# Kernel optimization log

Measured on AMD Instinct MI355X. Metric: run time of the kernel, lower is better.

## Reference

```python
import jax, jax.numpy as jnp
import numpy as np

RH, RW = 40, 64          # render image height/width
SAM_HW = 64              # SAM ViT-H feature map spatial size
FEAT_DIM = 17            # voxel_feature_dim
GAUSSIAN_SEM_WEIGHT = 1.0


def nearest_resize(x, oh, ow):
    # torch F.interpolate mode='nearest': idx = floor(out_idx * in/out)
    ih, iw = x.shape[-2], x.shape[-1]
    ri = jnp.floor(jnp.arange(oh) * (ih / oh)).astype(jnp.int32)
    ci = jnp.floor(jnp.arange(ow) * (iw / ow)).astype(jnp.int32)
    return x[..., ri, :][..., ci]


def bilinear_resize(x, oh, ow):
    # torch bilinear, align_corners=False (half-pixel centers)
    ih, iw = x.shape[-2], x.shape[-1]
    def axis(isz, osz):
        src = (jnp.arange(osz, dtype=x.dtype) + 0.5) * (isz / osz) - 0.5
        i0 = jnp.clip(jnp.floor(src), 0, isz - 1).astype(jnp.int32)
        i1 = jnp.clip(i0 + 1, 0, isz - 1)
        w = jnp.clip(src - i0.astype(x.dtype), 0.0, 1.0)
        return i0, i1, w
    r0, r1, wr = axis(ih, oh)
    c0, c1, wc = axis(iw, ow)
    xr = x[..., r0, :] * (1 - wr)[:, None] + x[..., r1, :] * wr[:, None]
    return xr[..., c0] * (1 - wc) + xr[..., c1] * wc


def quat_to_rot(q):  # q: [N,4] normalized (w,x,y,z)
    w, x, y, z = q[:, 0], q[:, 1], q[:, 2], q[:, 3]
    R = jnp.stack([
        1 - 2 * (y * y + z * z), 2 * (x * y - w * z), 2 * (x * z + w * y),
        2 * (x * y + w * z), 1 - 2 * (x * x + z * z), 2 * (y * z - w * x),
        2 * (x * z - w * y), 2 * (y * z + w * x), 1 - 2 * (x * x + y * y)], -1)
    return R.reshape(-1, 3, 3)


def sam_proj(x, W1, b1, g1, be1, W2, b2, g2, be2, W3, b3):
    # Linear -> LayerNorm -> LeakyReLU (x2) -> Linear, all on last dim
    def ln(h, g, b):
        mu = h.mean(-1, keepdims=True)
        var = ((h - mu) ** 2).mean(-1, keepdims=True)
        return (h - mu) / jnp.sqrt(var + 1e-5) * g + b
    h = jax.nn.leaky_relu(ln(x @ W1.T + b1, g1, be1), 0.01)
    h = jax.nn.leaky_relu(ln(h @ W2.T + b2, g2, be2), 0.01)
    return h @ W3.T + b3


def render_feature_map(xyz, feats, opac, scal, quat, vm, intr):
    # Differentiable EWA Gaussian-splat feature rasterizer (3DGS-style math).
    N = xyz.shape[0]
    Rw, t = vm[:3, :3], vm[:3, 3]
    cam = xyz @ Rw.T + t                      # [N,3] camera coords
    x, y, z = cam[:, 0], cam[:, 1], cam[:, 2]
    fx, fy, cx, cy = intr[0], intr[1], intr[2], intr[3]
    zc = jnp.maximum(z, 1e-3)
    u = fx * x / zc + cx
    v = fy * y / zc + cy
    # 3D covariance Sigma = R S S^T R^T, transformed to camera then projected
    Rq = quat_to_rot(quat)
    M = Rq * scal[:, None, :]
    cov3 = M @ jnp.swapaxes(M, 1, 2)          # [N,3,3]
    covw = jnp.einsum('ij,njk,lk->nil', Rw, cov3, Rw)
    inv_z = 1.0 / zc
    zero = jnp.zeros_like(z)
    J = jnp.stack([
        jnp.stack([fx * inv_z, zero, -fx * x * inv_z ** 2], -1),
        jnp.stack([zero, fy * inv_z, -fy * y * inv_z ** 2], -1)], 1)  # [N,2,3]
    cov2 = jnp.einsum('nij,njk,nlk->nil', J, covw, J)
    a = cov2[:, 0, 0] + 0.3
    bq = cov2[:, 0, 1]
    cc = cov2[:, 1, 1] + 0.3
    det = a * cc - bq * bq
    A, Bc, Cc = cc / det, -bq / det, a / det   # conic (inverse 2D cov)
    xx, yy = jnp.meshgrid(jnp.arange(RW, dtype=xyz.dtype), jnp.arange(RH, dtype=xyz.dtype))
    px, py = xx.reshape(-1), yy.reshape(-1)    # [P]
    dx = u[:, None] - px[None, :]              # [N,P]
    dy = v[:, None] - py[None, :]
    power = -0.5 * (A[:, None] * dx * dx + Cc[:, None] * dy * dy) - Bc[:, None] * dx * dy
    alpha = jnp.minimum(0.99, opac * jnp.exp(jnp.minimum(power, 0.0)))
    alpha = alpha * (z > 0.2).astype(alpha.dtype)[:, None]
    # depth-sorted alpha compositing
    order = jnp.argsort(z)
    a_s = alpha[order]                         # [N,P]
    f_s = feats[order]                         # [N,C]
    T = jnp.concatenate([jnp.ones((1, a_s.shape[1]), a_s.dtype),
                         jnp.cumprod(1.0 - a_s, axis=0)[:-1]], axis=0)
    out = jnp.einsum('np,nc->cp', a_s * T, f_s)  # white_background=False -> bg 0
    return out.reshape(FEAT_DIM, RH, RW)


def _forward(voxel_feats, opacity, sam_embd, sam_features, sam_masks, viewmat,
             intrins, pc_xyz, scales, rots, W1, b1, g1, be1, W2, b2, g2, be2, W3, b3):
    B, C = viewmat.shape[0], viewmat.shape[1]
    scal = jnp.exp(scales)
    quat = rots / jnp.linalg.norm(rots, axis=-1, keepdims=True)
    proj = lambda x: sam_proj(x, W1, b1, g1, be1, W2, b2, g2, be2, W3, b3)
    loss_batch = 0.0
    for b in range(B):
        vf = voxel_feats[b].reshape(-1, FEAT_DIM)
        op = opacity[b].reshape(-1, 1)
        loss_c = 0.0
        for c in range(C):
            fmap = render_feature_map(pc_xyz, vf, op, scal, quat, viewmat[b, c], intrins[b, c])
            # use_sam: L1 between rendered map and projected SAM embedding
            se = nearest_resize(sam_embd[b, c], RH, RW)          # [256,RH,RW]
            sed = proj(se.transpose(1, 2, 0))                    # [RH,RW,17]
            loss_c = loss_c + jnp.abs(fmap.transpose(1, 2, 0) - sed).mean()
            # SAM mask contrastive loss
            sf = sam_features[b, c]                              # [256,64,64]
            ldf = proj(sf.reshape(256, -1).T).T.reshape(FEAT_DIM, SAM_HW, SAM_HW)
            masks = sam_masks[b, c]                              # [M,200,200]
            lsm = nearest_resize(masks, SAM_HW, SAM_HW)          # [M,64,64]
            proto = jnp.einsum('mhw,chw->mc', lsm, ldf)
            proto = proto / jnp.maximum(lsm.sum((1, 2)), 1e-6)[:, None]
            prob = jax.nn.sigmoid(jnp.einsum('mc,chw->mhw', proto, fmap))
            frm = bilinear_resize(masks, RH, RW)
            frm = jnp.where(frm <= 0.5, 0.0, frm)
            bce = frm * jnp.log(prob + 1e-8) + (1 - frm) * jnp.log(1 - prob + 1e-8)
            loss_c = loss_c - bce.mean()
        loss_batch = loss_batch + loss_c / C
    return loss_batch / B * GAUSSIAN_SEM_WEIGHT


def setup_inputs() -> dict:
    key = jax.random.key(0)
    ks = jax.random.split(key, 10)
    vs = 2.0
    gx1 = np.arange(-40.0, 40.0 + vs - 0.1, vs)
    gx = (gx1[:40] + gx1[1:41]) / 2
    gy = gx.copy()
    gz1 = np.arange(-2.4, 13.6 + vs - 0.1, vs)
    gz = (gz1[:8] + gz1[1:9]) / 2
    X, Y, Z = np.meshgrid(gx, gy, gz, indexing='ij')
    pc_xyz = np.stack([X, Y, Z], -1).reshape(-1, 3).astype(np.float32)
    N = pc_xyz.shape[0]  # 12800
    # regular grid: 3-NN mean squared dist = vs^2 -> scales = log(sqrt(vs^2))
    scales = np.full((N, 3), np.log(vs), np.float32)
    rots = np.zeros((N, 4), np.float32); rots[:, 0] = 1.0
    vm = np.zeros((1, 2, 4, 4), np.float32)
    vm[0, :, 0, 0] = vm[0, :, 1, 1] = vm[0, :, 2, 2] = vm[0, :, 3, 3] = 1.0
    vm[0, 0, :3, 3] = [0.0, 0.0, 60.0]
    vm[0, 1, :3, 3] = [2.0, -1.0, 62.0]
    intr = np.tile(np.array([32.0, 20.0, 32.0, 20.0], np.float32), (1, 2, 1))
    inp = {
        'voxel_feats': jax.random.normal(ks[0], (1, N, 17), jnp.float32) * 0.5,
        'opacity': jax.random.uniform(ks[1], (1, N, 1), jnp.float32) * 0.1,
        'sam_embd': jax.random.normal(ks[2], (1, 2, 256, 64, 64), jnp.float32),
        'sam_features': jax.random.normal(ks[3], (1, 2, 256, 64, 64), jnp.float32),
        'sam_masks': (jax.random.uniform(ks[4], (1, 2, 16, 200, 200)) < 0.3).astype(jnp.float32),
        'viewmat': jnp.asarray(vm), 'intrins': jnp.asarray(intr),
        'pc_xyz': jnp.asarray(pc_xyz), 'scales': jnp.asarray(scales), 'rots': jnp.asarray(rots),
        'W1': jax.random.normal(ks[5], (64, 256), jnp.float32) * 0.05,
        'b1': jnp.zeros((64,), jnp.float32),
        'g1': jnp.ones((64,), jnp.float32), 'be1': jnp.zeros((64,), jnp.float32),
        'W2': jax.random.normal(ks[6], (64, 64), jnp.float32) * 0.1,
        'b2': jnp.zeros((64,), jnp.float32),
        'g2': jnp.ones((64,), jnp.float32), 'be2': jnp.zeros((64,), jnp.float32),
        'W3': jax.random.normal(ks[7], (17, 64), jnp.float32) * 0.1,
        'b3': jnp.zeros((17,), jnp.float32),
    }
    return inp


def reference(voxel_feats, opacity, sam_embd, sam_features, sam_masks, viewmat,
              intrins, pc_xyz, scales, rots, W1, b1, g1, be1, W2, b2, g2, be2, W3, b3):
    return _forward(voxel_feats, opacity, sam_embd, sam_features, sam_masks, viewmat,
                    intrins, pc_xyz, scales, rots, W1, b1, g1, be1, W2, b2, g2, be2, W3, b3)
```

## Files before the change

### kernel.cpp

```cpp
#include <hip/hip_runtime.h>
#include <math.h>

#define NPTS   12800
#define P_PIX  2560
#define NC     128
#define CHUNK  100
#define NRG    10
#define RANK_CHUNK 800
#define RT     4
#define MLP_PITCH 264

typedef short short8 __attribute__((ext_vector_type(8)));
typedef float f32x4 __attribute__((ext_vector_type(4)));
typedef float f32x2 __attribute__((ext_vector_type(2)));

__device__ __forceinline__ unsigned short f2bf(float f) {
    unsigned int u = __float_as_uint(f);
    u += 0x7fffu + ((u >> 16) & 1u);
    return (unsigned short)(u >> 16);
}

__device__ __forceinline__ float pack2h(float a, float b) {
    union { float f; _Float16 h[2]; } c;
    c.h[0] = (_Float16)a; c.h[1] = (_Float16)b;
    return c.f;
}
__device__ __forceinline__ float2 unpk2h(float w) {
    union { float f; _Float16 h[2]; } c; c.f = w;
    return make_float2((float)c.h[0], (float)c.h[1]);
}

__global__ __launch_bounds__(256) void prep_kernel(
    const float* __restrict__ xyz, const float* __restrict__ scales,
    const float* __restrict__ rots, const float* __restrict__ opacity,
    const float* __restrict__ viewmat, const float* __restrict__ intrins,
    unsigned long long* __restrict__ keys,
    float* __restrict__ pu, float* __restrict__ pv, float* __restrict__ prad,
    float* __restrict__ phA, float* __restrict__ phC, float* __restrict__ pnB,
    float* __restrict__ pop, int* __restrict__ rnk, float* __restrict__ out, int N) {
    int cam = blockIdx.y;
    int i = blockIdx.x * 256 + threadIdx.x;
    if (i >= N) return;
    int idx = cam * N + i;
    rnk[idx] = 0;
    if (idx == 0) out[0] = 0.0f;
    const float* vm = viewmat + cam * 16;
    const float* it = intrins + cam * 4;
    float fx = it[0], fy = it[1], cx = it[2], cy = it[3];
    float R00 = vm[0], R01 = vm[1], R02 = vm[2], t0 = vm[3];
    float R10 = vm[4], R11 = vm[5], R12 = vm[6], t1 = vm[7];
    float R20 = vm[8], R21 = vm[9], R22 = vm[10], t2 = vm[11];
    float X = xyz[i * 3], Y = xyz[i * 3 + 1], Z = xyz[i * 3 + 2];
    float x = R00 * X + R01 * Y + R02 * Z + t0;
    float y = R10 * X + R11 * Y + R12 * Z + t1;
    float z = R20 * X + R21 * Y + R22 * Z + t2;
    float zc = fmaxf(z, 0.001f);
    float iz = 1.0f / zc;
    float u = fx * x * iz + cx;
    float v = fy * y * iz + cy;
    float qw = rots[i * 4], qx = rots[i * 4 + 1], qy = rots[i * 4 + 2], qz = rots[i * 4 + 3];
    float qn = 1.0f / sqrtf(qw * qw + qx * qx + qy * qy + qz * qz);
    qw *= qn; qx *= qn; qy *= qn; qz *= qn;
    float s0 = expf(scales[i * 3]), s1 = expf(scales[i * 3 + 1]), s2 = expf(scales[i * 3 + 2]);
    float Rq[3][3] = {
        {1 - 2 * (qy * qy + qz * qz), 2 * (qx * qy - qw * qz), 2 * (qx * qz + qw * qy)},
        {2 * (qx * qy + qw * qz), 1 - 2 * (qx * qx + qz * qz), 2 * (qy * qz - qw * qx)},
        {2 * (qx * qz - qw * qy), 2 * (qy * qz + qw * qx), 1 - 2 * (qx * qx + qy * qy)}};
    float M[3][3];
    #pragma unroll
    for (int r = 0; r < 3; ++r) { M[r][0] = Rq[r][0] * s0; M[r][1] = Rq[r][1] * s1; M[r][2] = Rq[r][2] * s2; }
    float c3[3][3];
    #pragma unroll
    for (int a = 0; a < 3; ++a)
        #pragma unroll
        for (int b = 0; b < 3; ++b)
            c3[a][b] = M[a][0] * M[b][0] + M[a][1] * M[b][1] + M[a][2] * M[b][2];
    float Rw[3][3] = {{R00, R01, R02}, {R10, R11, R12}, {R20, R21, R22}};
    float Wt[3][3];
    #pragma unroll
    for (int a = 0; a < 3; ++a)
        #pragma unroll
        for (int b = 0; b < 3; ++b)
            Wt[a][b] = Rw[a][0] * c3[0][b] + Rw[a][1] * c3[1][b] + Rw[a][2] * c3[2][b];
    float cw[3][3];
    #pragma unroll
    for (int a = 0; a < 3; ++a)
        #pragma unroll
        for (int b = 0; b < 3; ++b)
            cw[a][b] = Wt[a][0] * Rw[b][0] + Wt[a][1] * Rw[b][1] + Wt[a][2] * Rw[b][2];
    float j00 = fx * iz, j02 = -fx * x * iz * iz;
    float j11 = fy * iz, j12 = -fy * y * iz * iz;
    float c00 = j00 * j00 * cw[0][0] + 2.0f * j00 * j02 * cw[0][2] + j02 * j02 * cw[2][2];
    float c01 = j00 * j11 * cw[0][1] + j00 * j12 * cw[0][2] + j02 * j11 * cw[2][1] + j02 * j12 * cw[2][2];
    float c11 = j11 * j11 * cw[1][1] + 2.0f * j11 * j12 * cw[1][2] + j12 * j12 * cw[2][2];
    float a = c00 + 0.3f, bq = c01, cc = c11 + 0.3f;
    float det = a * cc - bq * bq;
    float A = cc / det, Bc = -bq / det, Cc = a / det;
    float lmin = 0.5f * ((A + Cc) - sqrtf((A - Cc) * (A - Cc) + 4.0f * Bc * Bc));
    lmin = fmaxf(lmin, 1e-20f);
    float opv = (z > 0.2f) ? opacity[i] : 0.0f;
    float rad = -1.0f;
    if (opv > 0.0f) {
        float tcut = logf(opv) + 18.42f;
        if (tcut > 0.0f) rad = sqrtf(2.0f * tcut / lmin);
    }
    pu[idx] = u; pv[idx] = v; prad[idx] = rad;
    phA[idx] = -0.5f * A; phC[idx] = -0.5f * Cc; pnB[idx] = -Bc;
    pop[idx] = opv;
    unsigned int zb = __float_as_uint(z);
    zb = (zb & 0x80000000u) ? ~zb : (zb | 0x80000000u);
    keys[idx] = ((unsigned long long)zb << 32) | (unsigned int)i;
}

__global__ __launch_bounds__(256) void rank_kernel(const unsigned long long* __restrict__ keys,
                                                   int* __restrict__ rnk, int N) {
    __shared__ unsigned long long sk[RANK_CHUNK];
    int cam = blockIdx.z;
    const unsigned long long* K = keys + (size_t)cam * N;
    int jbase = blockIdx.y * RANK_CHUNK;
    int jcnt = min(RANK_CHUNK, N - jbase);
    for (int t = threadIdx.x; t < jcnt; t += 256) sk[t] = K[jbase + t];
    __syncthreads();
    int i0 = blockIdx.x * (256 * RT) + threadIdx.x;
    unsigned long long ki[RT];
    int cnt[RT];
    #pragma unroll
    for (int t = 0; t < RT; ++t) {
        int i = i0 + t * 256;
        ki[t] = (i < N) ? K[i] : 0xFFFFFFFFFFFFFFFFull;
        cnt[t] = 0;
    }
    #pragma unroll 4
    for (int j = 0; j < jcnt; ++j) {
        unsigned long long kj = sk[j];
        #pragma unroll
        for (int t = 0; t < RT; ++t) cnt[t] += (kj < ki[t]) ? 1 : 0;
    }
    #pragma unroll
    for (int t = 0; t < RT; ++t) {
        int i = i0 + t * 256;
        if (i < N && cnt[t]) atomicAdd(rnk + (size_t)cam * N + i, cnt[t]);
    }
}

__global__ __launch_bounds__(256) void scatter_kernel(
    const int* __restrict__ rnk,
    const float* __restrict__ pu, const float* __restrict__ pv, const float* __restrict__ prad,
    const float* __restrict__ phA, const float* __restrict__ phC, const float* __restrict__ pnB,
    const float* __restrict__ pop,
    const float* __restrict__ feats, float* __restrict__ rec, float2* __restrict__ vr, int N) {
    int cam = blockIdx.y;
    int i = blockIdx.x * 256 + threadIdx.x;
    if (i >= N) return;
    int idx = cam * N + i;
    int r = rnk[idx];
    float* d = rec + ((size_t)cam * N + r) * 16;
    d[0] = pu[idx]; d[1] = pv[idx];
    d[2] = pack2h(phA[idx], phC[idx]);
    d[3] = pack2h(pnB[idx], pop[idx]);
    const float* f = feats + (size_t)i * 17;
    #pragma unroll
    for (int j = 0; j < 8; ++j) d[4 + j] = pack2h(f[2 * j], f[2 * j + 1]);
    d[12] = pack2h(f[16], 0.0f);
    d[13] = 0.0f; d[14] = 0.0f; d[15] = 0.0f;
    vr[(size_t)cam * N + r] = make_float2(pv[idx], prad[idx]);
}

__global__ __launch_bounds__(256) void expand_kernel(const float2* __restrict__ vr,
                                                     const float* __restrict__ rec,
                                                     float* __restrict__ cstream,
                                                     int* __restrict__ cnts, int N) {
    int gid = blockIdx.x * 4 + (threadIdx.x >> 6);
    int lane = threadIdx.x & 63;
    int cam = gid / (NC * NRG);
    int rem = gid - cam * (NC * NRG);
    int ch = rem / NRG, rg = rem - ch * NRG;
    const float2* V = vr + (size_t)cam * N + ch * CHUNK;
    const float4* R = (const float4*)(rec + ((size_t)cam * N + ch * CHUNK) * 16);
    float4* S = (float4*)(cstream + (size_t)gid * CHUNK * 16);
    float cy = (float)(rg * 4) + 1.5f;
    int cnt = 0;
    #pragma unroll
    for (int g = 0; g < CHUNK; g += 64) {
        int n = g + lane;
        bool pass = false;
        if (n < CHUNK) {
            float2 t = V[n];
            pass = fabsf(t.x - cy) <= t.y + 2.01f;
        }
        unsigned long long mask = __ballot(pass);
        int pre = __popcll(mask & ((1ull << lane) - 1ull));
        if (pass) {
            int pos = cnt + pre;
            S[pos * 4 + 0] = R[n * 4 + 0];
            S[pos * 4 + 1] = R[n * 4 + 1];
            S[pos * 4 + 2] = R[n * 4 + 2];
            S[pos * 4 + 3] = R[n * 4 + 3];
        }
        cnt += __popcll(mask);
    }
    if (lane == 0) cnts[gid] = cnt;
}

__global__ __launch_bounds__(64) void splat_kernel(const float* __restrict__ cstream,
                                                   const int* __restrict__ cnts,
                                                   float* __restrict__ partT,
                                                   unsigned short* __restrict__ partS, int N) {
    __shared__ __align__(16) float4 sRec[CHUNK * 4];
    int rg = blockIdx.x, ch = blockIdx.y, cam = blockIdx.z;
    int lane = threadIdx.x;
    int lid = (cam * NC + ch) * NRG + rg;
    int cnt = cnts[lid];
    const float4* S = (const float4*)(cstream + (size_t)lid * CHUNK * 16);
    for (int t = lane; t < cnt * 4; t += 64) sRec[t] = S[t];
    __syncthreads();
    int r0 = rg * 4;
    float px = (float)lane, py0 = (float)r0;
    float T0 = 1.0f, T1 = 1.0f, T2 = 1.0f, T3 = 1.0f;
    f32x2 accA[17], accB[17];
    #pragma unroll
    for (int c = 0; c < 17; ++c) { accA[c] = (f32x2){0.f, 0.f}; accB[c] = (f32x2){0.f, 0.f}; }
    const float* sRf = (const float*)sRec;
    for (int i = 0; i < cnt; ++i) {
        const float4* rp = sRec + i * 4;
        float4 q0 = rp[0];
        float2 g0 = unpk2h(q0.z);
        float2 g1 = unpk2h(q0.w);
        float dx = q0.x - px;
        float dy = q0.y - py0;
        float ta = (g0.x * dx) * dx;
        float tb = g1.x * dx;
        float h2 = g0.y + g0.y;
        float p0 = fmaf(dy, fmaf(g0.y, dy, tb), ta);
        float e = fmaf(-h2, dy, g0.y - tb);
        float p1 = p0 + e; e += h2;
        float p2 = p1 + e; e += h2;
        float p3 = p2 + e;
        float a0 = fminf(0.99f, g1.y * __expf(fminf(p0, 0.0f)));
        float a1 = fminf(0.99f, g1.y * __expf(fminf(p1, 0.0f)));
        float a2 = fminf(0.99f, g1.y * __expf(fminf(p2, 0.0f)));
        float a3 = fminf(0.99f, g1.y * __expf(fminf(p3, 0.0f)));
        f32x2 wA = (f32x2){a0 * T0, a1 * T1};
        f32x2 wB = (f32x2){a2 * T2, a3 * T3};
        T0 = fmaf(-T0, a0, T0); T1 = fmaf(-T1, a1, T1);
        T2 = fmaf(-T2, a2, T2); T3 = fmaf(-T3, a3, T3);
        float4 q1 = rp[1], q2 = rp[2];
        float q3x = sRf[i * 16 + 12];
        float2 f01 = unpk2h(q1.x), f23 = unpk2h(q1.y), f45 = unpk2h(q1.z), f67 = unpk2h(q1.w);
        float2 f89 = unpk2h(q2.x), fab = unpk2h(q2.y), fcd = unpk2h(q2.z), fef = unpk2h(q2.w);
        float2 fg_ = unpk2h(q3x);
        accA[0]  += wA * f01.x;  accB[0]  += wB * f01.x;
        accA[1]  += wA * f01.y;  accB[1]  += wB * f01.y;
        accA[2]  += wA * f23.x;  accB[2]  += wB * f23.x;
        accA[3]  += wA * f23.y;  accB[3]  += wB * f23.y;
        accA[4]  += wA * f45.x;  accB[4]  += wB * f45.x;
        accA[5]  += wA * f45.y;  accB[5]  += wB * f45.y;
        accA[6]  += wA * f67.x;  accB[6]  += wB * f67.x;
        accA[7]  += wA * f67.y;  accB[7]  += wB * f67.y;
        accA[8]  += wA * f89.x;  accB[8]  += wB * f89.x;
        accA[9]  += wA * f89.y;  accB[9]  += wB * f89.y;
        accA[10] += wA * fab.x;  accB[10] += wB * fab.x;
        accA[11] += wA * fab.y;  accB[11] += wB * fab.y;
        accA[12] += wA * fcd.x;  accB[12] += wB * fcd.x;
        accA[13] += wA * fcd.y;  accB[13] += wB * fcd.y;
        accA[14] += wA * fef.x;  accB[14] += wB * fef.x;
        accA[15] += wA * fef.y;  accB[15] += wB * fef.y;
        accA[16] += wA * fg_.x;  accB[16] += wB * fg_.x;
    }
    size_t cbase = (size_t)(cam * NC + ch);
    size_t p0i = (size_t)r0 * 64 + lane;
    partT[cbase * P_PIX + p0i]       = T0;
    partT[cbase * P_PIX + p0i + 64]  = T1;
    partT[cbase * P_PIX + p0i + 128] = T2;
    partT[cbase * P_PIX + p0i + 192] = T3;
    _Float16* pS = (_Float16*)partS;
    #pragma unroll
    for (int c = 0; c < 17; ++c) {
        size_t b = (cbase * 17 + c) * P_PIX + p0i;
        pS[b]       = (_Float16)accA[c][0];
        pS[b + 64]  = (_Float16)accA[c][1];
        pS[b + 128] = (_Float16)accB[c][0];
        pS[b + 192] = (_Float16)accB[c][1];
    }
}

__global__ __launch_bounds__(256) void combine_kernel(const float* __restrict__ partT,
                                                      const unsigned short* __restrict__ partS,
                                                      float* __restrict__ fmap) {
    int idx = blockIdx.x * 256 + threadIdx.x;
    if (idx >= 2 * 17 * P_PIX) return;
    int p = idx % P_PIX;
    int rem = idx / P_PIX;
    int c = rem % 17;
    int cam = rem / 17;
    const _Float16* pS = (const _Float16*)partS;
    float acc = 0.0f, Tp = 1.0f;
    #pragma unroll 8
    for (int k = 0; k < NC; ++k) {
        size_t cb = (size_t)(cam * NC + k);
        float Tk = partT[cb * P_PIX + p];
        float S = (float)pS[(cb * 17 + c) * P_PIX + p];
        acc = fmaf(Tp, S, acc);
        Tp *= Tk;
    }
    fmap[((size_t)cam * 17 + c) * P_PIX + p] = acc;
}

__global__ __launch_bounds__(256, 2) void mlp_kernel(
    const float* __restrict__ embd, const float* __restrict__ sfeat,
    const float* __restrict__ W1, const float* __restrict__ b1,
    const float* __restrict__ g1, const float* __restrict__ be1,
    const float* __restrict__ W2, const float* __restrict__ b2,
    const float* __restrict__ g2, const float* __restrict__ be2,
    const float* __restrict__ W3, const float* __restrict__ b3,
    float* __restrict__ sed, float* __restrict__ ldf) {
    __shared__ __align__(16) unsigned short smem[2 * 64 * MLP_PITCH];
    unsigned short* sX = smem;
    unsigned short* sW = smem + 64 * MLP_PITCH;
    int tid = threadIdx.x, lane = tid & 63, wv = tid >> 6;
    int m = lane & 15, kq = lane >> 4, q4 = kq * 4;
    int tile = blockIdx.x;
    const float* xbase;
    if (tile < 80) {
        int cam = tile / 40; int r = tile - cam * 40;
        int ri = (r * 8) / 5;
        xbase = embd + (size_t)cam * 256 * 4096 + ri * 64;
    } else {
        int tt = tile - 80; int cam = tt >> 6;
        xbase = sfeat + (size_t)cam * 256 * 4096 + (tt & 63) * 64;
    }
    const float4* xf4 = (const float4*)xbase;
    for (int idx = tid; idx < 4096; idx += 256) {
        int k = idx >> 4, q = idx & 15;
        float4 xv = xf4[(size_t)k * 1024 + q];
        int r = q * 4;
        sX[(r + 0) * MLP_PITCH + k] = f2bf(xv.x);
        sX[(r + 1) * MLP_PITCH + k] = f2bf(xv.y);
        sX[(r + 2) * MLP_PITCH + k] = f2bf(xv.z);
        sX[(r + 3) * MLP_PITCH + k] = f2bf(xv.w);
    }
    const float4* wf4 = (const float4*)W1;
    for (int idx = tid; idx < 4096; idx += 256) {
        float4 wvv = wf4[idx];
        int n = idx >> 6, kk = (idx & 63) * 4;
        uint2 pk;
        pk.x = (unsigned int)f2bf(wvv.x) | ((unsigned int)f2bf(wvv.y) << 16);
        pk.y = (unsigned int)f2bf(wvv.z) | ((unsigned int)f2bf(wvv.w) << 16);
        *(uint2*)&sW[n * MLP_PITCH + kk] = pk;
    }
    float b1v[4], g1v[4], be1v[4], b2v[4], g2v[4], be2v[4];
    #pragma unroll
    for (int nt = 0; nt < 4; ++nt) {
        int c = nt * 16 + m;
        b1v[nt] = b1[c]; g1v[nt] = g1[c]; be1v[nt] = be1[c];
        b2v[nt] = b2[c]; g2v[nt] = g2[c]; be2v[nt] = be2[c];
    }
    __syncthreads();
    f32x4 acc[4];
    #pragma unroll
    for (int nt = 0; nt < 4; ++nt) acc[nt] = (f32x4){0.f, 0.f, 0.f, 0.f};
    const unsigned short* aptr = sX + (wv * 16 + m) * MLP_PITCH + kq * 8;
    const unsigned short* bptr = sW + m * MLP_PITCH + kq * 8;
    #pragma unroll
    for (int ks = 0; ks < 8; ++ks) {
        short8 af = *(const short8*)(aptr + ks * 32);
        #pragma unroll
        for (int nt = 0; nt < 4; ++nt) {
            short8 bf = *(const short8*)(bptr + nt * 16 * MLP_PITCH + ks * 32);
            acc[nt] = __builtin_amdgcn_mfma_f32_16x16x32_bf16(af, bf, acc[nt], 0, 0, 0);
        }
    }
    __syncthreads();
    unsigned short* hbuf  = smem + wv * 16 * 72;
    unsigned short* hbuf2 = smem + (4 + wv) * 16 * 72;
    unsigned short* W2b = sW;
    unsigned short* W3b = sW + 64 * 72;
    for (int i = tid; i < 4096; i += 256)
        W2b[(i >> 6) * 72 + (i & 63)] = f2bf(W2[i]);
    for (int i = tid; i < 2048; i += 256) {
        int n = i >> 6, k = i & 63;
        W3b[n * 72 + k] = (n < 17) ? f2bf(W3[n * 64 + k]) : 0;
    }
    #pragma unroll
    for (int rg = 0; rg < 4; ++rg) {
        float h0 = acc[0][rg] + b1v[0], h1 = acc[1][rg] + b1v[1];
        float h2 = acc[2][rg] + b1v[2], h3 = acc[3][rg] + b1v[3];
        float s = (h0 + h1) + (h2 + h3);
        s += __shfl_xor(s, 1); s += __shfl_xor(s, 2);
        s += __shfl_xor(s, 4); s += __shfl_xor(s, 8);
        float mu = s * (1.0f / 64.0f);
        float d0 = h0 - mu, d1 = h1 - mu, d2 = h2 - mu, d3 = h3 - mu;
        float vs = (d0 * d0 + d1 * d1) + (d2 * d2 + d3 * d3);
        vs += __shfl_xor(vs, 1); vs += __shfl_xor(vs, 2);
        vs += __shfl_xor(vs, 4); vs += __shfl_xor(vs, 8);
        float rstd = 1.0f / sqrtf(vs * (1.0f / 64.0f) + 1e-5f);
        float hn0 = d0 * rstd * g1v[0] + be1v[0]; hn0 = fmaxf(hn0, 0.01f * hn0);
        float hn1 = d1 * rstd * g1v[1] + be1v[1]; hn1 = fmaxf(hn1, 0.01f * hn1);
        float hn2 = d2 * rstd * g1v[2] + be1v[2]; hn2 = fmaxf(hn2, 0.01f * hn2);
        float hn3 = d3 * rstd * g1v[3] + be1v[3]; hn3 = fmaxf(hn3, 0.01f * hn3);
        int rr = (q4 + rg) * 72 + m;
        hbuf[rr] = f2bf(hn0); hbuf[rr + 16] = f2bf(hn1);
        hbuf[rr + 32] = f2bf(hn2); hbuf[rr + 48] = f2bf(hn3);
    }
    __syncthreads();
    f32x4 acc2[4];
    #pragma unroll
    for (int nt = 0; nt < 4; ++nt) acc2[nt] = (f32x4){0.f, 0.f, 0.f, 0.f};
    const unsigned short* a2p = hbuf + m * 72 + kq * 8;
    #pragma unroll
    for (int ks = 0; ks < 2; ++ks) {
        short8 af = *(const short8*)(a2p + ks * 32);
        #pragma unroll
        for (int nt = 0; nt < 4; ++nt) {
            short8 bf = *(const short8*)(W2b + (nt * 16 + m) * 72 + kq * 8 + ks * 32);
            acc2[nt] = __builtin_amdgcn_mfma_f32_16x16x32_bf16(af, bf, acc2[nt], 0, 0, 0);
        }
    }
    #pragma unroll
    for (int rg = 0; rg < 4; ++rg) {
        float h0 = acc2[0][rg] + b2v[0], h1 = acc2[1][rg] + b2v[1];
        float h2 = acc2[2][rg] + b2v[2], h3 = acc2[3][rg] + b2v[3];
        float s = (h0 + h1) + (h2 + h3);
        s += __shfl_xor(s, 1); s += __shfl_xor(s, 2);
        s += __shfl_xor(s, 4); s += __shfl_xor(s, 8);
        float mu = s * (1.0f / 64.0f);
        float d0 = h0 - mu, d1 = h1 - mu, d2 = h2 - mu, d3 = h3 - mu;
        float vs = (d0 * d0 + d1 * d1) + (d2 * d2 + d3 * d3);
        vs += __shfl_xor(vs, 1); vs += __shfl_xor(vs, 2);
        vs += __shfl_xor(vs, 4); vs += __shfl_xor(vs, 8);
        float rstd = 1.0f / sqrtf(vs * (1.0f / 64.0f) + 1e-5f);
        float hn0 = d0 * rstd * g2v[0] + be2v[0]; hn0 = fmaxf(hn0, 0.01f * hn0);
        float hn1 = d1 * rstd * g2v[1] + be2v[1]; hn1 = fmaxf(hn1, 0.01f * hn1);
        float hn2 = d2 * rstd * g2v[2] + be2v[2]; hn2 = fmaxf(hn2, 0.01f * hn2);
        float hn3 = d3 * rstd * g2v[3] + be2v[3]; hn3 = fmaxf(hn3, 0.01f * hn3);
        int rr = (q4 + rg) * 72 + m;
        hbuf2[rr] = f2bf(hn0); hbuf2[rr + 16] = f2bf(hn1);
        hbuf2[rr + 32] = f2bf(hn2); hbuf2[rr + 48] = f2bf(hn3);
    }
    f32x4 acc3[2];
    acc3[0] = (f32x4){0.f, 0.f, 0.f, 0.f};
    acc3[1] = (f32x4){0.f, 0.f, 0.f, 0.f};
    const unsigned short* a3p = hbuf2 + m * 72 + kq * 8;
    #pragma unroll
    for (int ks = 0; ks < 2; ++ks) {
        short8 af = *(const short8*)(a3p + ks * 32);
        #pragma unroll
        for (int nt = 0; nt < 2; ++nt) {
            short8 bf = *(const short8*)(W3b + (nt * 16 + m) * 72 + kq * 8 + ks * 32);
            acc3[nt] = __builtin_amdgcn_mfma_f32_16x16x32_bf16(af, bf, acc3[nt], 0, 0, 0);
        }
    }
    #pragma unroll
    for (int nt = 0; nt < 2; ++nt) {
        int c = nt * 16 + m;
        if (c < 17) {
            float b3v = b3[c];
            #pragma unroll
            for (int rg = 0; rg < 4; ++rg) {
                int row = tile * 64 + wv * 16 + q4 + rg;
                float val = acc3[nt][rg] + b3v;
                if (row < 5120) {
                    int cam = row / 2560; int p = row - cam * 2560;
                    sed[((size_t)cam * 2560 + p) * 17 + c] = val;
                } else {
                    int rr = row - 5120; int cam = rr >> 12; int t = rr & 4095;
                    ldf[((size_t)cam * 17 + c) * 4096 + t] = val;
                }
            }
        }
    }
}

__global__ __launch_bounds__(256) void proto_kernel(const float* __restrict__ masks,
                                                    const float* __restrict__ ldf,
                                                    float* __restrict__ proto) {
    int cam = blockIdx.y, m = blockIdx.x;
    const float* M = masks + ((size_t)cam * 16 + m) * 40000;
    float acc[18];
    #pragma unroll
    for (int j = 0; j < 18; ++j) acc[j] = 0.0f;
    for (int t = threadIdx.x; t < 4096; t += 256) {
        int h = t >> 6, w = t & 63;
        int rh = (h * 25) >> 3, rw = (w * 25) >> 3;
        float lv = M[rh * 200 + rw];
        if (lv != 0.0f) {
            acc[17] += lv;
            const float* L = ldf + (size_t)cam * 17 * 4096 + t;
            #pragma unroll
            for (int c = 0; c < 17; ++c) acc[c] = fmaf(lv, L[(size_t)c * 4096], acc[c]);
        }
    }
    __shared__ float red[4][18];
    int lane = threadIdx.x & 63, wv = threadIdx.x >> 6;
    #pragma unroll
    for (int j = 0; j < 18; ++j) {
        float v = acc[j];
        #pragma unroll
        for (int o = 32; o; o >>= 1) v += __shfl_xor(v, o);
        if (lane == 0) red[wv][j] = v;
    }
    __syncthreads();
    if (threadIdx.x < 17) {
        float sacc = red[0][threadIdx.x] + red[1][threadIdx.x] + red[2][threadIdx.x] + red[3][threadIdx.x];
        float ms = red[0][17] + red[1][17] + red[2][17] + red[3][17];
        proto[((size_t)cam * 16 + m) * 17 + threadIdx.x] = sacc / fmaxf(ms, 1e-6f);
    }
}

__device__ __forceinline__ void block_atomic_add(float v, float* target) {
    #pragma unroll
    for (int o = 32; o; o >>= 1) v += __shfl_xor(v, o);
    __shared__ float sred[4];
    int lane = threadIdx.x & 63, wv = threadIdx.x >> 6;
    if (lane == 0) sred[wv] = v;
    __syncthreads();
    if (threadIdx.x == 0) atomicAdd(target, sred[0] + sred[1] + sred[2] + sred[3]);
}

__global__ __launch_bounds__(256) void bce_kernel(const float* __restrict__ masks,
                                                  const float* __restrict__ proto,
                                                  const float* __restrict__ fmap,
                                                  const float* __restrict__ sed,
                                                  float* __restrict__ out) {
    int idx = blockIdx.x * 256 + threadIdx.x;
    int p = idx % P_PIX;
    int rem = idx / P_PIX;
    int m = rem & 15, cam = rem >> 4;
    const float* pr = proto + ((size_t)cam * 16 + m) * 17;
    float f[17];
    #pragma unroll
    for (int c = 0; c < 17; ++c) f[c] = fmap[((size_t)cam * 17 + c) * P_PIX + p];
    float sdot = 0;
    #pragma unroll
    for (int c = 0; c < 17; ++c) sdot = fmaf(pr[c], f[c], sdot);
    float prob = 1.0f / (1.0f + __expf(-sdot));
    int px = p & 63, py = p >> 6;
    float src_r = (py + 0.5f) * 5.0f - 0.5f;
    float src_c = (px + 0.5f) * 3.125f - 0.5f;
    int r0 = (int)fminf(fmaxf(floorf(src_r), 0.0f), 199.0f);
    int r1 = min(r0 + 1, 199);
    float wr = fminf(fmaxf(src_r - (float)r0, 0.0f), 1.0f);
    int c0 = (int)fminf(fmaxf(floorf(src_c), 0.0f), 199.0f);
    int c1 = min(c0 + 1, 199);
    float wc = fminf(fmaxf(src_c - (float)c0, 0.0f), 1.0f);
    const float* M = masks + ((size_t)cam * 16 + m) * 40000;
    float v00 = M[r0 * 200 + c0], v01 = M[r0 * 200 + c1];
    float v10 = M[r1 * 200 + c0], v11 = M[r1 * 200 + c1];
    float xr0 = v00 * (1.0f - wr) + v10 * wr;
    float xr1 = v01 * (1.0f - wr) + v11 * wr;
    float frm = xr0 * (1.0f - wc) + xr1 * wc;
    frm = (frm <= 0.5f) ? 0.0f : frm;
    float bce = frm * __logf(prob + 1e-8f) + (1.0f - frm) * __logf(1.0f - prob + 1e-8f);
    float val = bce * (-1.0f / (16.0f * 2560.0f * 2.0f));
    if (m == 0) {
        float ssum = 0.0f;
        const float* sp = sed + ((size_t)cam * P_PIX + p) * 17;
        #pragma unroll
        for (int c = 0; c < 17; ++c) ssum += fabsf(f[c] - sp[c]);
        val += ssum * (1.0f / (43520.0f * 2.0f));
    }
    block_atomic_add(val, out);
}

extern "C" void kernel_launch(void* const* d_in, const int* in_sizes, int n_in,
                              void* d_out, int out_size, void* d_ws, size_t ws_size,
                              hipStream_t stream) {
    const float* voxel_feats = (const float*)d_in[0];
    const float* opacity     = (const float*)d_in[1];
    const float* sam_embd    = (const float*)d_in[2];
    const float* sam_features= (const float*)d_in[3];
    const float* sam_masks   = (const float*)d_in[4];
    const float* viewmat     = (const float*)d_in[5];
    const float* intrins     = (const float*)d_in[6];
    const float* pc_xyz      = (const float*)d_in[7];
    const float* scales      = (const float*)d_in[8];
    const float* rots        = (const float*)d_in[9];
    const float* W1 = (const float*)d_in[10], *b1 = (const float*)d_in[11];
    const float* g1 = (const float*)d_in[12], *be1 = (const float*)d_in[13];
    const float* W2 = (const float*)d_in[14], *b2 = (const float*)d_in[15];
    const float* g2 = (const float*)d_in[16], *be2 = (const float*)d_in[17];
    const float* W3 = (const float*)d_in[18], *b3 = (const float*)d_in[19];
    float* out = (float*)d_out;
    const int N = in_sizes[7] / 3;

    char* w = (char*)d_ws;
    size_t off = 0;
    auto alloc = [&](size_t bytes) -> void* {
        off = (off + 255) & ~(size_t)255;
        void* p = w + off; off += bytes; return p;
    };
    int* rnk  = (int*)alloc((size_t)2 * N * sizeof(int));
    unsigned long long* keys = (unsigned long long*)alloc((size_t)2 * N * 8);
    float* params = (float*)alloc((size_t)7 * 2 * N * 4);
    float* pu  = params,           *pv  = params + 2 * N,  *prad = params + 4 * N;
    float* phA = params + 6 * N,   *phC = params + 8 * N,  *pnB  = params + 10 * N;
    float* pop = params + 12 * N;
    float* rec   = (float*)alloc((size_t)2 * N * 16 * 4);
    float2* vr   = (float2*)alloc((size_t)2 * N * 8);
    float* cstream = (float*)alloc((size_t)2 * NC * NRG * CHUNK * 16 * 4);
    int* cnts = (int*)alloc((size_t)2 * NC * NRG * sizeof(int));
    float* partT = (float*)alloc((size_t)2 * NC * P_PIX * 4);
    unsigned short* partS = (unsigned short*)alloc((size_t)2 * NC * 17 * P_PIX * 2);
    float* fmap  = (float*)alloc((size_t)2 * 17 * P_PIX * 4);
    float* sed   = (float*)alloc((size_t)2 * P_PIX * 17 * 4);
    float* ldf   = (float*)alloc((size_t)2 * 17 * 4096 * 4);
    float* proto = (float*)alloc((size_t)2 * 16 * 17 * 4);

    dim3 gprep((N + 255) / 256, 2);
    prep_kernel<<<gprep, 256, 0, stream>>>(pc_xyz, scales, rots, opacity, viewmat, intrins,
                                           keys, pu, pv, prad, phA, phC, pnB, pop, rnk, out, N);
    dim3 grank((N + 256 * RT - 1) / (256 * RT), (N + RANK_CHUNK - 1) / RANK_CHUNK, 2);
    rank_kernel<<<grank, 256, 0, stream>>>(keys, rnk, N);
    scatter_kernel<<<gprep, 256, 0, stream>>>(rnk, pu, pv, prad, phA, phC, pnB, pop,
                                              voxel_feats, rec, vr, N);
    expand_kernel<<<2 * NC * NRG / 4, 256, 0, stream>>>(vr, rec, cstream, cnts, N);
    dim3 gsplat(NRG, NC, 2);
    splat_kernel<<<gsplat, 64, 0, stream>>>(cstream, cnts, partT, partS, N);
    mlp_kernel<<<208, 256, 0, stream>>>(sam_embd, sam_features, W1, b1, g1, be1,
                                        W2, b2, g2, be2, W3, b3, sed, ldf);
    combine_kernel<<<(2 * 17 * P_PIX + 255) / 256, 256, 0, stream>>>(partT, partS, fmap);
    dim3 gproto(16, 2);
    proto_kernel<<<gproto, 256, 0, stream>>>(sam_masks, ldf, proto);
    bce_kernel<<<(2 * 16 * P_PIX) / 256, 256, 0, stream>>>(sam_masks, proto, fmap, sed, out);
}
```

Measured before the change: 248.5 us.

## Fuse scatter with MLP, expand into splat, combine with proto; fp16 splat accumulation

Several changes land together. The scatter kernel is merged into the MLP kernel as extra blocks, and the expand pass is folded into the splat kernel, which now compacts records in shared memory. The combine and proto kernels become one launch, the rank chunk size is halved, and the splat accumulators switch from fp32 to packed fp16 math. These cut launch count and the cstream round trip through global memory. In exchange, fp16 accumulation lowers precision, and the cull margin is tightened from 2.01 to 1.51, which could drop contributions.

```diff
diff --git a/kernel.cpp b/kernel.cpp
--- a/kernel.cpp
+++ b/kernel.cpp
@@ -6,13 +6,16 @@
 #define NC     128
 #define CHUNK  100
 #define NRG    10
-#define RANK_CHUNK 800
+#define RANK_CHUNK 400
 #define RT     4
 #define MLP_PITCH 264
 
 typedef short short8 __attribute__((ext_vector_type(8)));
 typedef float f32x4 __attribute__((ext_vector_type(4)));
 typedef float f32x2 __attribute__((ext_vector_type(2)));
+typedef _Float16 h16x2 __attribute__((ext_vector_type(2)));
+
+union F2H { float f; h16x2 h; unsigned short s[2]; };
 
 __device__ __forceinline__ unsigned short f2bf(float f) {
     unsigned int u = __float_as_uint(f);
@@ -143,183 +146,45 @@
     }
 }
 
-__global__ __launch_bounds__(256) void scatter_kernel(
+__global__ __launch_bounds__(256, 2) void scatter_mlp_kernel(
     const int* __restrict__ rnk,
     const float* __restrict__ pu, const float* __restrict__ pv, const float* __restrict__ prad,
     const float* __restrict__ phA, const float* __restrict__ phC, const float* __restrict__ pnB,
-    const float* __restrict__ pop,
-    const float* __restrict__ feats, float* __restrict__ rec, float2* __restrict__ vr, int N) {
-    int cam = blockIdx.y;
-    int i = blockIdx.x * 256 + threadIdx.x;
-    if (i >= N) return;
-    int idx = cam * N + i;
-    int r = rnk[idx];
-    float* d = rec + ((size_t)cam * N + r) * 16;
-    d[0] = pu[idx]; d[1] = pv[idx];
-    d[2] = pack2h(phA[idx], phC[idx]);
-    d[3] = pack2h(pnB[idx], pop[idx]);
-    const float* f = feats + (size_t)i * 17;
-    #pragma unroll
-    for (int j = 0; j < 8; ++j) d[4 + j] = pack2h(f[2 * j], f[2 * j + 1]);
-    d[12] = pack2h(f[16], 0.0f);
-    d[13] = 0.0f; d[14] = 0.0f; d[15] = 0.0f;
-    vr[(size_t)cam * N + r] = make_float2(pv[idx], prad[idx]);
-}
-
-__global__ __launch_bounds__(256) void expand_kernel(const float2* __restrict__ vr,
-                                                     const float* __restrict__ rec,
-                                                     float* __restrict__ cstream,
-                                                     int* __restrict__ cnts, int N) {
-    int gid = blockIdx.x * 4 + (threadIdx.x >> 6);
-    int lane = threadIdx.x & 63;
-    int cam = gid / (NC * NRG);
-    int rem = gid - cam * (NC * NRG);
-    int ch = rem / NRG, rg = rem - ch * NRG;
-    const float2* V = vr + (size_t)cam * N + ch * CHUNK;
-    const float4* R = (const float4*)(rec + ((size_t)cam * N + ch * CHUNK) * 16);
-    float4* S = (float4*)(cstream + (size_t)gid * CHUNK * 16);
-    float cy = (float)(rg * 4) + 1.5f;
-    int cnt = 0;
-    #pragma unroll
-    for (int g = 0; g < CHUNK; g += 64) {
-        int n = g + lane;
-        bool pass = false;
-        if (n < CHUNK) {
-            float2 t = V[n];
-            pass = fabsf(t.x - cy) <= t.y + 2.01f;
-        }
-        unsigned long long mask = __ballot(pass);
-        int pre = __popcll(mask & ((1ull << lane) - 1ull));
-        if (pass) {
-            int pos = cnt + pre;
-            S[pos * 4 + 0] = R[n * 4 + 0];
-            S[pos * 4 + 1] = R[n * 4 + 1];
-            S[pos * 4 + 2] = R[n * 4 + 2];
-            S[pos * 4 + 3] = R[n * 4 + 3];
-        }
-        cnt += __popcll(mask);
-    }
-    if (lane == 0) cnts[gid] = cnt;
-}
-
-__global__ __launch_bounds__(64) void splat_kernel(const float* __restrict__ cstream,
-                                                   const int* __restrict__ cnts,
-                                                   float* __restrict__ partT,
-                                                   unsigned short* __restrict__ partS, int N) {
-    __shared__ __align__(16) float4 sRec[CHUNK * 4];
-    int rg = blockIdx.x, ch = blockIdx.y, cam = blockIdx.z;
-    int lane = threadIdx.x;
-    int lid = (cam * NC + ch) * NRG + rg;
-    int cnt = cnts[lid];
-    const float4* S = (const float4*)(cstream + (size_t)lid * CHUNK * 16);
-    for (int t = lane; t < cnt * 4; t += 64) sRec[t] = S[t];
-    __syncthreads();
-    int r0 = rg * 4;
-    float px = (float)lane, py0 = (float)r0;
-    float T0 = 1.0f, T1 = 1.0f, T2 = 1.0f, T3 = 1.0f;
-    f32x2 accA[17], accB[17];
-    #pragma unroll
-    for (int c = 0; c < 17; ++c) { accA[c] = (f32x2){0.f, 0.f}; accB[c] = (f32x2){0.f, 0.f}; }
-    const float* sRf = (const float*)sRec;
-    for (int i = 0; i < cnt; ++i) {
-        const float4* rp = sRec + i * 4;
-        float4 q0 = rp[0];
-        float2 g0 = unpk2h(q0.z);
-        float2 g1 = unpk2h(q0.w);
-        float dx = q0.x - px;
-        float dy = q0.y - py0;
-        float ta = (g0.x * dx) * dx;
-        float tb = g1.x * dx;
-        float h2 = g0.y + g0.y;
-        float p0 = fmaf(dy, fmaf(g0.y, dy, tb), ta);
-        float e = fmaf(-h2, dy, g0.y - tb);
-        float p1 = p0 + e; e += h2;
-        float p2 = p1 + e; e += h2;
-        float p3 = p2 + e;
-        float a0 = fminf(0.99f, g1.y * __expf(fminf(p0, 0.0f)));
-        float a1 = fminf(0.99f, g1.y * __expf(fminf(p1, 0.0f)));
-        float a2 = fminf(0.99f, g1.y * __expf(fminf(p2, 0.0f)));
-        float a3 = fminf(0.99f, g1.y * __expf(fminf(p3, 0.0f)));
-        f32x2 wA = (f32x2){a0 * T0, a1 * T1};
-        f32x2 wB = (f32x2){a2 * T2, a3 * T3};
-        T0 = fmaf(-T0, a0, T0); T1 = fmaf(-T1, a1, T1);
-        T2 = fmaf(-T2, a2, T2); T3 = fmaf(-T3, a3, T3);
-        float4 q1 = rp[1], q2 = rp[2];
-        float q3x = sRf[i * 16 + 12];
-        float2 f01 = unpk2h(q1.x), f23 = unpk2h(q1.y), f45 = unpk2h(q1.z), f67 = unpk2h(q1.w);
-        float2 f89 = unpk2h(q2.x), fab = unpk2h(q2.y), fcd = unpk2h(q2.z), fef = unpk2h(q2.w);
-        float2 fg_ = unpk2h(q3x);
-        accA[0]  += wA * f01.x;  accB[0]  += wB * f01.x;
-        accA[1]  += wA * f01.y;  accB[1]  += wB * f01.y;
-        accA[2]  += wA * f23.x;  accB[2]  += wB * f23.x;
-        accA[3]  += wA * f23.y;  accB[3]  += wB * f23.y;
-        accA[4]  += wA * f45.x;  accB[4]  += wB * f45.x;
-        accA[5]  += wA * f45.y;  accB[5]  += wB * f45.y;
-        accA[6]  += wA * f67.x;  accB[6]  += wB * f67.x;
-        accA[7]  += wA * f67.y;  accB[7]  += wB * f67.y;
-        accA[8]  += wA * f89.x;  accB[8]  += wB * f89.x;
-        accA[9]  += wA * f89.y;  accB[9]  += wB * f89.y;
-        accA[10] += wA * fab.x;  accB[10] += wB * fab.x;
-        accA[11] += wA * fab.y;  accB[11] += wB * fab.y;
-        accA[12] += wA * fcd.x;  accB[12] += wB * fcd.x;
-        accA[13] += wA * fcd.y;  accB[13] += wB * fcd.y;
-        accA[14] += wA * fef.x;  accB[14] += wB * fef.x;
-        accA[15] += wA * fef.y;  accB[15] += wB * fef.y;
-        accA[16] += wA * fg_.x;  accB[16] += wB * fg_.x;
-    }
-    size_t cbase = (size_t)(cam * NC + ch);
-    size_t p0i = (size_t)r0 * 64 + lane;
-    partT[cbase * P_PIX + p0i]       = T0;
-    partT[cbase * P_PIX + p0i + 64]  = T1;
-    partT[cbase * P_PIX + p0i + 128] = T2;
-    partT[cbase * P_PIX + p0i + 192] = T3;
-    _Float16* pS = (_Float16*)partS;
-    #pragma unroll
-    for (int c = 0; c < 17; ++c) {
-        size_t b = (cbase * 17 + c) * P_PIX + p0i;
-        pS[b]       = (_Float16)accA[c][0];
-        pS[b + 64]  = (_Float16)accA[c][1];
-        pS[b + 128] = (_Float16)accB[c][0];
-        pS[b + 192] = (_Float16)accB[c][1];
-    }
-}
-
-__global__ __launch_bounds__(256) void combine_kernel(const float* __restrict__ partT,
-                                                      const unsigned short* __restrict__ partS,
-                                                      float* __restrict__ fmap) {
-    int idx = blockIdx.x * 256 + threadIdx.x;
-    if (idx >= 2 * 17 * P_PIX) return;
-    int p = idx % P_PIX;
-    int rem = idx / P_PIX;
-    int c = rem % 17;
-    int cam = rem / 17;
-    const _Float16* pS = (const _Float16*)partS;
-    float acc = 0.0f, Tp = 1.0f;
-    #pragma unroll 8
-    for (int k = 0; k < NC; ++k) {
-        size_t cb = (size_t)(cam * NC + k);
-        float Tk = partT[cb * P_PIX + p];
-        float S = (float)pS[(cb * 17 + c) * P_PIX + p];
-        acc = fmaf(Tp, S, acc);
-        Tp *= Tk;
-    }
-    fmap[((size_t)cam * 17 + c) * P_PIX + p] = acc;
-}
-
-__global__ __launch_bounds__(256, 2) void mlp_kernel(
+    const float* __restrict__ pop, const float* __restrict__ feats,
+    float* __restrict__ rec, float2* __restrict__ vr,
     const float* __restrict__ embd, const float* __restrict__ sfeat,
     const float* __restrict__ W1, const float* __restrict__ b1,
     const float* __restrict__ g1, const float* __restrict__ be1,
     const float* __restrict__ W2, const float* __restrict__ b2,
     const float* __restrict__ g2, const float* __restrict__ be2,
     const float* __restrict__ W3, const float* __restrict__ b3,
-    float* __restrict__ sed, float* __restrict__ ldf) {
+    float* __restrict__ sed, float* __restrict__ ldf, int N) {
     __shared__ __align__(16) unsigned short smem[2 * 64 * MLP_PITCH];
+    int bid = blockIdx.x;
+    int tid = threadIdx.x;
+    if (bid < 100) {
+        int cam = bid / 50;
+        int i = (bid % 50) * 256 + tid;
+        if (i >= N) return;
+        int idx = cam * N + i;
+        int r = rnk[idx];
+        float* d = rec + ((size_t)cam * N + r) * 16;
+        d[0] = pu[idx]; d[1] = pv[idx];
+        d[2] = pack2h(phA[idx], phC[idx]);
+        d[3] = pack2h(pnB[idx], pop[idx]);
+        const float* f = feats + (size_t)i * 17;
+        #pragma unroll
+        for (int j = 0; j < 8; ++j) d[4 + j] = pack2h(f[2 * j], f[2 * j + 1]);
+        d[12] = pack2h(f[16], 0.0f);
+        d[13] = 0.0f; d[14] = 0.0f; d[15] = 0.0f;
+        vr[(size_t)cam * N + r] = make_float2(pv[idx], prad[idx]);
+        return;
+    }
     unsigned short* sX = smem;
     unsigned short* sW = smem + 64 * MLP_PITCH;
-    int tid = threadIdx.x, lane = tid & 63, wv = tid >> 6;
+    int lane = tid & 63, wv = tid >> 6;
     int m = lane & 15, kq = lane >> 4, q4 = kq * 4;
-    int tile = blockIdx.x;
+    int tile = bid - 100;
     const float* xbase;
     if (tile < 80) {
         int cam = tile / 40; int r = tile - cam * 40;
@@ -471,10 +336,134 @@
     }
 }
 
-__global__ __launch_bounds__(256) void proto_kernel(const float* __restrict__ masks,
-                                                    const float* __restrict__ ldf,
-                                                    float* __restrict__ proto) {
-    int cam = blockIdx.y, m = blockIdx.x;
+__global__ __launch_bounds__(64) void splat_kernel(const float* __restrict__ rec,
+                                                   const float2* __restrict__ vr,
+                                                   float* __restrict__ partT,
+                                                   unsigned short* __restrict__ partS, int N) {
+    __shared__ __align__(16) float4 sRaw[CHUNK * 4];
+    __shared__ __align__(16) float4 sCmp[CHUNK * 4];
+    __shared__ unsigned char sIdx[CHUNK];
+    int rg = blockIdx.x, ch = blockIdx.y, cam = blockIdx.z;
+    int lane = threadIdx.x;
+    const float4* src = (const float4*)(rec + ((size_t)cam * N + ch * CHUNK) * 16);
+    for (int t = lane; t < CHUNK * 4; t += 64) sRaw[t] = src[t];
+    const float2* V = vr + (size_t)cam * N + ch * CHUNK;
+    float cy = (float)(rg * 4) + 1.5f;
+    int cnt = 0;
+    for (int g = 0; g < CHUNK; g += 64) {
+        int n = g + lane;
+        bool pass = false;
+        if (n < CHUNK) {
+            float2 t = V[n];
+            pass = fabsf(t.x - cy) <= t.y + 1.51f;
+        }
+        unsigned long long mask = __ballot(pass);
+        int pre = __popcll(mask & ((1ull << lane) - 1ull));
+        if (pass) sIdx[cnt + pre] = (unsigned char)n;
+        cnt += __popcll(mask);
+    }
+    __syncthreads();
+    for (int l = lane; l < cnt; l += 64) {
+        int n = sIdx[l];
+        sCmp[l * 4 + 0] = sRaw[n * 4 + 0];
+        sCmp[l * 4 + 1] = sRaw[n * 4 + 1];
+        sCmp[l * 4 + 2] = sRaw[n * 4 + 2];
+        sCmp[l * 4 + 3] = sRaw[n * 4 + 3];
+    }
+    __syncthreads();
+    int r0 = rg * 4;
+    float px = (float)lane, py0 = (float)r0;
+    float T0 = 1.0f, T1 = 1.0f, T2 = 1.0f, T3 = 1.0f;
+    h16x2 acc[4][9];
+    #pragma unroll
+    for (int r = 0; r < 4; ++r)
+        #pragma unroll
+        for (int j = 0; j < 9; ++j) acc[r][j] = (h16x2){(_Float16)0.f, (_Float16)0.f};
+    const float* sRf = (const float*)sCmp;
+    for (int i = 0; i < cnt; ++i) {
+        const float4* rp = sCmp + i * 4;
+        float4 q0 = rp[0];
+        float2 g0 = unpk2h(q0.z);
+        float2 g1 = unpk2h(q0.w);
+        float dx = q0.x - px;
+        float dy = q0.y - py0;
+        float ta = (g0.x * dx) * dx;
+        float tb = g1.x * dx;
+        float h2 = g0.y + g0.y;
+        float p0 = fmaf(dy, fmaf(g0.y, dy, tb), ta);
+        float e = fmaf(-h2, dy, g0.y - tb);
+        float p1 = p0 + e; e += h2;
+        float p2 = p1 + e; e += h2;
+        float p3 = p2 + e;
+        float a0 = fminf(0.99f, g1.y * __expf(fminf(p0, 0.0f)));
+        float a1 = fminf(0.99f, g1.y * __expf(fminf(p1, 0.0f)));
+        float a2 = fminf(0.99f, g1.y * __expf(fminf(p2, 0.0f)));
+        float a3 = fminf(0.99f, g1.y * __expf(fminf(p3, 0.0f)));
+        float w0 = a0 * T0, w1 = a1 * T1, w2 = a2 * T2, w3 = a3 * T3;
+        T0 = fmaf(-T0, a0, T0); T1 = fmaf(-T1, a1, T1);
+        T2 = fmaf(-T2, a2, T2); T3 = fmaf(-T3, a3, T3);
+        h16x2 wh[4];
+        wh[0] = (h16x2){(_Float16)w0, (_Float16)w0};
+        wh[1] = (h16x2){(_Float16)w1, (_Float16)w1};
+        wh[2] = (h16x2){(_Float16)w2, (_Float16)w2};
+        wh[3] = (h16x2){(_Float16)w3, (_Float16)w3};
+        float4 q1 = rp[1], q2 = rp[2];
+        float fg = sRf[i * 16 + 12];
+        F2H f[9];
+        f[0].f = q1.x; f[1].f = q1.y; f[2].f = q1.z; f[3].f = q1.w;
+        f[4].f = q2.x; f[5].f = q2.y; f[6].f = q2.z; f[7].f = q2.w;
+        f[8].f = fg;
+        #pragma unroll
+        for (int r = 0; r < 4; ++r)
+            #pragma unroll
+            for (int j = 0; j < 9; ++j)
+                acc[r][j] += wh[r] * f[j].h;
+    }
+    size_t cbase = (size_t)(cam * NC + ch);
+    size_t p0i = (size_t)r0 * 64 + lane;
+    partT[cbase * P_PIX + p0i]       = T0;
+    partT[cbase * P_PIX + p0i + 64]  = T1;
+    partT[cbase * P_PIX + p0i + 128] = T2;
+    partT[cbase * P_PIX + p0i + 192] = T3;
+    #pragma unroll
+    for (int r = 0; r < 4; ++r) {
+        #pragma unroll
+        for (int c = 0; c < 17; ++c) {
+            F2H v; v.h = acc[r][c >> 1];
+            partS[(cbase * 17 + c) * P_PIX + p0i + (size_t)r * 64] = v.s[c & 1];
+        }
+    }
+}
+
+__global__ __launch_bounds__(256) void combine_proto_kernel(const float* __restrict__ partT,
+                                                            const unsigned short* __restrict__ partS,
+                                                            const float* __restrict__ masks,
+                                                            const float* __restrict__ ldf,
+                                                            float* __restrict__ fmap,
+                                                            float* __restrict__ proto) {
+    __shared__ float red[4][18];
+    int bid = blockIdx.x;
+    if (bid < 340) {
+        int idx = bid * 256 + threadIdx.x;
+        int p = idx % P_PIX;
+        int rem = idx / P_PIX;
+        int c = rem % 17;
+        int cam = rem / 17;
+        const _Float16* pS = (const _Float16*)partS;
+        float acc = 0.0f, Tp = 1.0f;
+        #pragma unroll 8
+        for (int k = 0; k < NC; ++k) {
+            size_t cb = (size_t)(cam * NC + k);
+            float Tk = partT[cb * P_PIX + p];
+            float S = (float)pS[(cb * 17 + c) * P_PIX + p];
+            acc = fmaf(Tp, S, acc);
+            Tp *= Tk;
+        }
+        fmap[((size_t)cam * 17 + c) * P_PIX + p] = acc;
+        return;
+    }
+    int t0 = bid - 340;
+    int m = t0 & 15, cam = t0 >> 4;
     const float* M = masks + ((size_t)cam * 16 + m) * 40000;
     float acc[18];
     #pragma unroll
@@ -490,7 +479,6 @@
             for (int c = 0; c < 17; ++c) acc[c] = fmaf(lv, L[(size_t)c * 4096], acc[c]);
         }
     }
-    __shared__ float red[4][18];
     int lane = threadIdx.x & 63, wv = threadIdx.x >> 6;
     #pragma unroll
     for (int j = 0; j < 18; ++j) {
@@ -597,8 +585,6 @@
     float* pop = params + 12 * N;
     float* rec   = (float*)alloc((size_t)2 * N * 16 * 4);
     float2* vr   = (float2*)alloc((size_t)2 * N * 8);
-    float* cstream = (float*)alloc((size_t)2 * NC * NRG * CHUNK * 16 * 4);
-    int* cnts = (int*)alloc((size_t)2 * NC * NRG * sizeof(int));
     float* partT = (float*)alloc((size_t)2 * NC * P_PIX * 4);
     unsigned short* partS = (unsigned short*)alloc((size_t)2 * NC * 17 * P_PIX * 2);
     float* fmap  = (float*)alloc((size_t)2 * 17 * P_PIX * 4);
@@ -611,15 +597,12 @@
                                            keys, pu, pv, prad, phA, phC, pnB, pop, rnk, out, N);
     dim3 grank((N + 256 * RT - 1) / (256 * RT), (N + RANK_CHUNK - 1) / RANK_CHUNK, 2);
     rank_kernel<<<grank, 256, 0, stream>>>(keys, rnk, N);
-    scatter_kernel<<<gprep, 256, 0, stream>>>(rnk, pu, pv, prad, phA, phC, pnB, pop,
-                                              voxel_feats, rec, vr, N);
-    expand_kernel<<<2 * NC * NRG / 4, 256, 0, stream>>>(vr, rec, cstream, cnts, N);
+    scatter_mlp_kernel<<<308, 256, 0, stream>>>(rnk, pu, pv, prad, phA, phC, pnB, pop,
+                                                voxel_feats, rec, vr,
+                                                sam_embd, sam_features, W1, b1, g1, be1,
+                                                W2, b2, g2, be2, W3, b3, sed, ldf, N);
     dim3 gsplat(NRG, NC, 2);
-    splat_kernel<<<gsplat, 64, 0, stream>>>(cstream, cnts, partT, partS, N);
-    mlp_kernel<<<208, 256, 0, stream>>>(sam_embd, sam_features, W1, b1, g1, be1,
-                                        W2, b2, g2, be2, W3, b3, sed, ldf);
-    combine_kernel<<<(2 * 17 * P_PIX + 255) / 256, 256, 0, stream>>>(partT, partS, fmap);
-    dim3 gproto(16, 2);
-    proto_kernel<<<gproto, 256, 0, stream>>>(sam_masks, ldf, proto);
+    splat_kernel<<<gsplat, 64, 0, stream>>>(rec, vr, partT, partS, N);
+    combine_proto_kernel<<<372, 256, 0, stream>>>(partT, partS, sam_masks, ldf, fmap, proto);
     bce_kernel<<<(2 * 16 * P_PIX) / 256, 256, 0, stream>>>(sam_masks, proto, fmap, sed, out);
 }
```

Result: faster. 211.6 us (-14.8%).
